# Performance work log

Measured on AMD Instinct MI355X. Metric: run time of the kernel, lower is better.

The kernel has to match this reference:

```python
import jax, jax.numpy as jnp
import numpy as np

B, N, H, W, P = 32, 6, 512, 512, 512
SCALE, ASPECT, MIN_PH = 0.5, 1.0, 60.0


def setup_inputs() -> dict:
    key = jax.random.key(0)
    k1, k2, k3, k4, k5, k6 = jax.random.split(key, 6)
    images = jax.random.normal(k1, (B, H, W, 3), jnp.float32)
    patch = jax.random.normal(k2, (P, P, 3), jnp.float32)
    # person bboxes (ymin, xmin, ymax, xmax) in pixels, fully inside the image
    hsz = jax.random.uniform(k3, (B, N), jnp.float32, 120.0, 400.0)
    wsz = jax.random.uniform(k4, (B, N), jnp.float32, 120.0, 400.0)
    ymin = jax.random.uniform(k5, (B, N), jnp.float32) * (H - hsz)
    xmin = jax.random.uniform(k6, (B, N), jnp.float32) * (W - wsz)
    boxes = jnp.stack([ymin, xmin, ymin + hsz, xmin + wsz], axis=-1)
    return {"images": images, "boxes": boxes, "patch": patch}


def _patch_boxes(boxes):
    # Patcher.create: derive (ymin_patch, xmin_patch, patch_h, patch_w) from each bbox
    ymin, xmin, ymax, xmax = (boxes[..., 0], boxes[..., 1], boxes[..., 2], boxes[..., 3])
    h = ymax - ymin
    w = xmax - xmin
    pw = h * SCALE
    ph = ASPECT * pw
    oy = ymin + h * 0.5
    ox = xmin + w * 0.5
    yp = jnp.maximum(oy - ph * 0.5, 0.0)
    xp = jnp.maximum(ox - pw * 0.5, 0.0)
    yp = jnp.where(yp + ph > H, H - ph, yp)
    xp = jnp.where(xp + pw > W, W - pw, xp)
    valid = ph > MIN_PH  # ragged filter -> mask
    return jnp.stack([yp, xp, ph, pw], axis=-1), valid


def _paste_one(img, patch, box, valid):
    # fused gather(resize bilinear, half-pixel centers) + scatter of the patch into img
    Pn = patch.shape[0]
    b = box.astype(jnp.int32)  # tf.cast truncation
    y0b, x0b, h, w = b[0], b[1], b[2], b[3]
    hf = jnp.maximum(h, 1).astype(jnp.float32)
    wf = jnp.maximum(w, 1).astype(jnp.float32)
    dy = jnp.arange(img.shape[0]) - y0b
    dx = jnp.arange(img.shape[1]) - x0b
    sy = jnp.clip((dy.astype(jnp.float32) + 0.5) * (Pn / hf) - 0.5, 0.0, Pn - 1.0)
    sx = jnp.clip((dx.astype(jnp.float32) + 0.5) * (Pn / wf) - 0.5, 0.0, Pn - 1.0)
    yl = jnp.floor(sy).astype(jnp.int32); yh = jnp.minimum(yl + 1, Pn - 1); wy = sy - yl
    xl = jnp.floor(sx).astype(jnp.int32); xh = jnp.minimum(xl + 1, Pn - 1); wx = sx - xl
    # separable bilinear: rows [H, P, 3] then cols -> [H, W, 3]
    rows = patch[yl] * (1.0 - wy)[:, None, None] + patch[yh] * wy[:, None, None]
    val = rows[:, xl] * (1.0 - wx)[None, :, None] + rows[:, xh] * wx[None, :, None]
    inside = ((dy >= 0) & (dy < h))[:, None] & ((dx >= 0) & (dx < w))[None, :] & valid
    return jnp.where(inside[..., None], val, img)


def reference(images, boxes, patch):
    pboxes, valid = _patch_boxes(boxes)
    def step(imgs, xs):
        bx, v = xs  # [B,4], [B]
        imgs = jax.vmap(lambda im, b_, v_: _paste_one(im, patch, b_, v_))(imgs, bx, v)
        return imgs, None
    # sequential over patches (later patches overwrite earlier, as in the tf while_loop)
    out, _ = jax.lax.scan(step, images, (jnp.transpose(pboxes, (1, 0, 2)), valid.T))
    return out
```

## Files before the change

kernel.cpp:

```cpp
#include <hip/hip_runtime.h>


#define Bn 32
#define Nn 6
#define Hh 512
#define Ww 512
#define Pp 512

typedef float f32x4 __attribute__((ext_vector_type(4)));

__global__ __launch_bounds__(256) void patch_attack_kernel(
    const float* __restrict__ images,
    const float* __restrict__ boxes,
    const float* __restrict__ patch,
    float* __restrict__ out)
{
    __shared__ float lds[3072];

    const int tid   = threadIdx.x;
    const int chunk = blockIdx.x * 256 + tid;
    const int b     = chunk >> 16;
    const int rem   = chunk & 65535;
    const int y     = rem >> 7;
    const int x4    = (rem & 127) << 2;

    const float* __restrict__ bx = boxes + (size_t)b * Nn * 4;

    float r[12];
    bool cov[4] = {false, false, false, false};

    #pragma unroll
    for (int n = Nn - 1; n >= 0; --n) {
        const float ymin = bx[n * 4 + 0];
        const float xmin = bx[n * 4 + 1];
        const float ymax = bx[n * 4 + 2];
        const float xmax = bx[n * 4 + 3];
        const float h  = ymax - ymin;
        const float w  = xmax - xmin;
        const float pw = h * 0.5f;
        const float ph = 1.0f * pw;
        const float oy = ymin + h * 0.5f;
        const float ox = xmin + w * 0.5f;
        float yp = fmaxf(oy - ph * 0.5f, 0.0f);
        float xp = fmaxf(ox - pw * 0.5f, 0.0f);
        yp = (yp + ph > (float)Hh) ? ((float)Hh - ph) : yp;
        xp = (xp + pw > (float)Ww) ? ((float)Ww - pw) : xp;
        const bool valid = ph > 60.0f;

        const int y0b = (int)yp;
        const int x0b = (int)xp;
        const int hI  = (int)ph;
        const int wI  = (int)pw;
        const int dy  = y - y0b;

        if (!(valid && dy >= 0 && dy < hI)) continue;

        const float hf = (float)(hI > 1 ? hI : 1);
        const float wf = (float)(wI > 1 ? wI : 1);
        float sy = ((float)dy + 0.5f) * ((float)Pp / hf) - 0.5f;
        sy = fminf(fmaxf(sy, 0.0f), (float)(Pp - 1));
        const int   yl = (int)floorf(sy);
        const int   yh = (yl + 1 < Pp - 1) ? (yl + 1) : (Pp - 1);
        const float wy = sy - (float)yl;
        const float omwy = 1.0f - wy;
        const float winv = (float)Pp / wf;
        const float* __restrict__ rowl = patch + (size_t)yl * (Pp * 3);
        const float* __restrict__ rowh = patch + (size_t)yh * (Pp * 3);

        #pragma unroll
        for (int j = 0; j < 4; ++j) {
            if (cov[j]) continue;
            const int dx = x4 + j - x0b;
            if (dx < 0 || dx >= wI) continue;

            float sx = ((float)dx + 0.5f) * winv - 0.5f;
            sx = fminf(fmaxf(sx, 0.0f), (float)(Pp - 1));
            const int   xl = (int)floorf(sx);
            const int   xh = (xl + 1 < Pp - 1) ? (xl + 1) : (Pp - 1);
            const float wx = sx - (float)xl;
            const float omwx = 1.0f - wx;

            const float* __restrict__ pll = rowl + xl * 3;
            const float* __restrict__ plh = rowl + xh * 3;
            const float* __restrict__ phl = rowh + xl * 3;
            const float* __restrict__ phh = rowh + xh * 3;
            r[j * 3 + 0] = (pll[0] * omwy + phl[0] * wy) * omwx + (plh[0] * omwy + phh[0] * wy) * wx;
            r[j * 3 + 1] = (pll[1] * omwy + phl[1] * wy) * omwx + (plh[1] * omwy + phh[1] * wy) * wx;
            r[j * 3 + 2] = (pll[2] * omwy + phl[2] * wy) * omwx + (plh[2] * omwy + phh[2] * wy) * wx;
            cov[j] = true;
        }
        if (cov[0] & cov[1] & cov[2] & cov[3]) break;
    }

    if (!(cov[0] & cov[1] & cov[2] & cov[3])) {
        const f32x4* __restrict__ ip =
            (const f32x4*)(images + (size_t)chunk * 12);
        const f32x4 i0 = __builtin_nontemporal_load(ip + 0);
        const f32x4 i1 = __builtin_nontemporal_load(ip + 1);
        const f32x4 i2 = __builtin_nontemporal_load(ip + 2);
        const float img[12] = {i0.x, i0.y, i0.z, i0.w,
                               i1.x, i1.y, i1.z, i1.w,
                               i2.x, i2.y, i2.z, i2.w};
        #pragma unroll
        for (int j = 0; j < 4; ++j) {
            if (!cov[j]) {
                r[j * 3 + 0] = img[j * 3 + 0];
                r[j * 3 + 1] = img[j * 3 + 1];
                r[j * 3 + 2] = img[j * 3 + 2];
            }
        }
    }

    f32x4* __restrict__ lw = (f32x4*)(lds + tid * 12);
    f32x4 w0, w1, w2;
    w0.x = r[0];  w0.y = r[1];  w0.z = r[2];  w0.w = r[3];
    w1.x = r[4];  w1.y = r[5];  w1.z = r[6];  w1.w = r[7];
    w2.x = r[8];  w2.y = r[9];  w2.z = r[10]; w2.w = r[11];
    lw[0] = w0;
    lw[1] = w1;
    lw[2] = w2;

    __syncthreads();

    const size_t blk_f = (size_t)blockIdx.x * 3072;
    #pragma unroll
    for (int k = 0; k < 3; ++k) {
        const f32x4 v = *(const f32x4*)(lds + k * 1024 + tid * 4);
        __builtin_nontemporal_store(
            v, (f32x4*)(out + blk_f + (size_t)k * 1024 + (size_t)tid * 4));
    }
}

extern "C" void kernel_launch(void* const* d_in, const int* in_sizes, int n_in,
                              void* d_out, int out_size, void* d_ws, size_t ws_size,
                              hipStream_t stream) {
    const float* images = (const float*)d_in[0];
    const float* boxes  = (const float*)d_in[1];
    const float* patch  = (const float*)d_in[2];
    float* out = (float*)d_out;

    const int total_chunks = Bn * Hh * Ww / 4;
    const int block = 256;
    const int grid  = total_chunks / block;

    patch_attack_kernel<<<grid, block, 0, stream>>>(images, boxes, patch, out);
}
```

Baseline: 209.7 us.

## Resolve covering patch per pixel first, then batch vectorized bilinear gathers

Restructures the per-pixel loop so that it first records which patch covers each of the four pixels, along with its source offset and weights, without loading anything, and then issues all patch gathers together as wide unaligned vector loads. The row index is clamped to P-2 so the high neighbour always sits at a fixed byte offset. The batch index and the row index are hoisted into scalar registers with readfirstlane. The intent is to remove divergent, dependent scalar loads inside the loop and to expose memory-level parallelism. In exchange every lane loads patch data whenever any lane in the wave is covered, and the clamp at P-2 changes the interpolation only at the edge, where the weight works out to the same value.

Result: faster. 198.2 us (-5.5%).

```diff
diff --git a/kernel.cpp b/kernel.cpp
--- a/kernel.cpp
+++ b/kernel.cpp
@@ -8,6 +8,8 @@
 #define Pp 512
 
 typedef float f32x4 __attribute__((ext_vector_type(4)));
+typedef float f32x4u __attribute__((ext_vector_type(4), aligned(4)));
+typedef float f32x2u __attribute__((ext_vector_type(2), aligned(4)));
 
 __global__ __launch_bounds__(256) void patch_attack_kernel(
     const float* __restrict__ images,
@@ -19,15 +21,17 @@
 
     const int tid   = threadIdx.x;
     const int chunk = blockIdx.x * 256 + tid;
-    const int b     = chunk >> 16;
+    const int b     = __builtin_amdgcn_readfirstlane(chunk >> 16);
     const int rem   = chunk & 65535;
-    const int y     = rem >> 7;
+    const int y     = __builtin_amdgcn_readfirstlane(rem >> 7);
     const int x4    = (rem & 127) << 2;
 
-    const float* __restrict__ bx = boxes + (size_t)b * Nn * 4;
+    const float* __restrict__ bx = boxes + b * (Nn * 4);
 
-    float r[12];
-    bool cov[4] = {false, false, false, false};
+    int   bid[4]  = {-1, -1, -1, -1};
+    int   offL[4] = {0, 0, 0, 0};
+    float wxs[4]  = {0.f, 0.f, 0.f, 0.f};
+    float wys[4]  = {0.f, 0.f, 0.f, 0.f};
 
     #pragma unroll
     for (int n = Nn - 1; n >= 0; --n) {
@@ -59,56 +63,76 @@
         const float wf = (float)(wI > 1 ? wI : 1);
         float sy = ((float)dy + 0.5f) * ((float)Pp / hf) - 0.5f;
         sy = fminf(fmaxf(sy, 0.0f), (float)(Pp - 1));
-        const int   yl = (int)floorf(sy);
-        const int   yh = (yl + 1 < Pp - 1) ? (yl + 1) : (Pp - 1);
-        const float wy = sy - (float)yl;
-        const float omwy = 1.0f - wy;
+        int yl = (int)sy;
+        yl = (yl > Pp - 2) ? (Pp - 2) : yl;
+        const float wyv = sy - (float)yl;
         const float winv = (float)Pp / wf;
-        const float* __restrict__ rowl = patch + (size_t)yl * (Pp * 3);
-        const float* __restrict__ rowh = patch + (size_t)yh * (Pp * 3);
+        const int rl = yl * (Pp * 3 * 4);
 
         #pragma unroll
         for (int j = 0; j < 4; ++j) {
-            if (cov[j]) continue;
             const int dx = x4 + j - x0b;
-            if (dx < 0 || dx >= wI) continue;
-
             float sx = ((float)dx + 0.5f) * winv - 0.5f;
             sx = fminf(fmaxf(sx, 0.0f), (float)(Pp - 1));
-            const int   xl = (int)floorf(sx);
-            const int   xh = (xl + 1 < Pp - 1) ? (xl + 1) : (Pp - 1);
-            const float wx = sx - (float)xl;
-            const float omwx = 1.0f - wx;
-
-            const float* __restrict__ pll = rowl + xl * 3;
-            const float* __restrict__ plh = rowl + xh * 3;
-            const float* __restrict__ phl = rowh + xl * 3;
-            const float* __restrict__ phh = rowh + xh * 3;
-            r[j * 3 + 0] = (pll[0] * omwy + phl[0] * wy) * omwx + (plh[0] * omwy + phh[0] * wy) * wx;
-            r[j * 3 + 1] = (pll[1] * omwy + phl[1] * wy) * omwx + (plh[1] * omwy + phh[1] * wy) * wx;
-            r[j * 3 + 2] = (pll[2] * omwy + phl[2] * wy) * omwx + (plh[2] * omwy + phh[2] * wy) * wx;
-            cov[j] = true;
+            int xl = (int)sx;
+            xl = (xl > Pp - 2) ? (Pp - 2) : xl;
+            const float wxv = sx - (float)xl;
+            const bool hit = (dx >= 0) & (dx < wI) & (bid[j] < 0);
+            if (hit) {
+                bid[j]  = n;
+                offL[j] = rl + xl * 12;
+                wxs[j]  = wxv;
+                wys[j]  = wyv;
+            }
         }
-        if (cov[0] & cov[1] & cov[2] & cov[3]) break;
     }
 
-    if (!(cov[0] & cov[1] & cov[2] & cov[3])) {
-        const f32x4* __restrict__ ip =
-            (const f32x4*)(images + (size_t)chunk * 12);
-        const f32x4 i0 = __builtin_nontemporal_load(ip + 0);
-        const f32x4 i1 = __builtin_nontemporal_load(ip + 1);
-        const f32x4 i2 = __builtin_nontemporal_load(ip + 2);
-        const float img[12] = {i0.x, i0.y, i0.z, i0.w,
-                               i1.x, i1.y, i1.z, i1.w,
-                               i2.x, i2.y, i2.z, i2.w};
+    const bool c0 = bid[0] >= 0, c1 = bid[1] >= 0, c2 = bid[2] >= 0, c3 = bid[3] >= 0;
+    f32x4 i0 = {0.f, 0.f, 0.f, 0.f}, i1 = i0, i2 = i0;
+    if (!(c0 & c1 & c2 & c3)) {
+        const f32x4* __restrict__ ip = (const f32x4*)(images + (size_t)chunk * 12);
+        i0 = __builtin_nontemporal_load(ip + 0);
+        i1 = __builtin_nontemporal_load(ip + 1);
+        i2 = __builtin_nontemporal_load(ip + 2);
+    }
+
+    float pr[12] = {0.f, 0.f, 0.f, 0.f, 0.f, 0.f, 0.f, 0.f, 0.f, 0.f, 0.f, 0.f};
+    const char* __restrict__ pbytes = (const char*)patch;
+    if (__any(c0 | c1 | c2 | c3)) {
+        float A[4][6], Bv[4][6];
         #pragma unroll
         for (int j = 0; j < 4; ++j) {
-            if (!cov[j]) {
-                r[j * 3 + 0] = img[j * 3 + 0];
-                r[j * 3 + 1] = img[j * 3 + 1];
-                r[j * 3 + 2] = img[j * 3 + 2];
+            const f32x4u a0 = *(const f32x4u*)(pbytes + offL[j]);
+            const f32x2u a1 = *(const f32x2u*)(pbytes + offL[j] + 16);
+            const f32x4u b0 = *(const f32x4u*)(pbytes + offL[j] + 6144);
+            const f32x2u b1 = *(const f32x2u*)(pbytes + offL[j] + 6160);
+            A[j][0] = a0.x;  A[j][1] = a0.y;  A[j][2] = a0.z;
+            A[j][3] = a0.w;  A[j][4] = a1.x;  A[j][5] = a1.y;
+            Bv[j][0] = b0.x; Bv[j][1] = b0.y; Bv[j][2] = b0.z;
+            Bv[j][3] = b0.w; Bv[j][4] = b1.x; Bv[j][5] = b1.y;
+        }
+        #pragma unroll
+        for (int j = 0; j < 4; ++j) {
+            const float wyv = wys[j], wxv = wxs[j];
+            const float omy = 1.0f - wyv, omx = 1.0f - wxv;
+            #pragma unroll
+            for (int c = 0; c < 3; ++c) {
+                pr[j * 3 + c] = (A[j][c]     * omy + Bv[j][c]     * wyv) * omx
+                              + (A[j][3 + c] * omy + Bv[j][3 + c] * wyv) * wxv;
             }
         }
+    }
+
+    const float img[12] = {i0.x, i0.y, i0.z, i0.w,
+                           i1.x, i1.y, i1.z, i1.w,
+                           i2.x, i2.y, i2.z, i2.w};
+    float r[12];
+    #pragma unroll
+    for (int j = 0; j < 4; ++j) {
+        const bool cv = bid[j] >= 0;
+        r[j * 3 + 0] = cv ? pr[j * 3 + 0] : img[j * 3 + 0];
+        r[j * 3 + 1] = cv ? pr[j * 3 + 1] : img[j * 3 + 1];
+        r[j * 3 + 2] = cv ? pr[j * 3 + 2] : img[j * 3 + 2];
     }
 
     f32x4* __restrict__ lw = (f32x4*)(lds + tid * 12);
```
